# Optimization experiments

Hardware: AMD Instinct MI355X
Metric: run time of the kernel (lower is better)

The kernel has to match this reference:

```python
import jax, jax.numpy as jnp
import numpy as np

V, E, CIN, COUT, NH, HID = 8192, 2048, 128, 128, 4, 32
EPS = 1e-5

def _ln(x, g, b):
    m = x.mean(-1, keepdims=True)
    v = x.var(-1, keepdims=True)
    return (x - m) / jnp.sqrt(v + EPS) * g + b

def setup_inputs() -> dict:
    key = jax.random.key(0)
    ks = jax.random.split(key, 12)
    s = 0.05
    X = jax.random.normal(ks[0], (V, CIN), jnp.float32)
    H = jax.random.bernoulli(ks[1], 0.02, (V, E)).astype(jnp.float32)
    edge_features = jax.random.normal(ks[2], (E, COUT), jnp.float32)
    Wv = jax.random.normal(ks[3], (CIN, COUT), jnp.float32) * s
    bv = jnp.zeros((COUT,), jnp.float32)
    We = jax.random.normal(ks[4], (COUT, COUT), jnp.float32) * s
    be = jnp.zeros((COUT,), jnp.float32)
    vW1 = jax.random.normal(ks[5], (NH, CIN, HID), jnp.float32) * s
    vb1 = jnp.zeros((NH, HID), jnp.float32)
    vW2 = jax.random.normal(ks[6], (NH, HID), jnp.float32) * s
    vb2 = jnp.zeros((NH,), jnp.float32)
    eW1 = jax.random.normal(ks[7], (COUT, HID), jnp.float32) * s
    eb1 = jnp.zeros((HID,), jnp.float32)
    eW2 = jax.random.normal(ks[8], (HID,), jnp.float32) * s
    eb2 = jnp.zeros((), jnp.float32)
    Wc = jax.random.normal(ks[9], (NH * COUT, COUT), jnp.float32) * s
    bc = jnp.zeros((COUT,), jnp.float32)
    Wg = jax.random.normal(ks[10], (CIN + COUT, COUT), jnp.float32) * s
    bg = jnp.zeros((COUT,), jnp.float32)
    return dict(X=X, H=H, edge_features=edge_features, Wv=Wv, bv=bv, We=We, be=be,
                vW1=vW1, vb1=vb1, vW2=vW2, vb2=vb2, eW1=eW1, eb1=eb1, eW2=eW2, eb2=eb2,
                Wc=Wc, bc=bc,
                ln_e_g=jnp.ones((COUT,), jnp.float32), ln_e_b=jnp.zeros((COUT,), jnp.float32),
                ln_v_g=jnp.ones((COUT,), jnp.float32), ln_v_b=jnp.zeros((COUT,), jnp.float32),
                bn_g=jnp.ones((COUT,), jnp.float32), bn_b=jnp.zeros((COUT,), jnp.float32),
                Wg=Wg, bg=bg)

def reference(X, H, edge_features, Wv, bv, We, be, vW1, vb1, vW2, vb2,
              eW1, eb1, eW2, eb2, Wc, bc, ln_e_g, ln_e_b, ln_v_g, ln_v_b,
              bn_g, bn_b, Wg, bg):
    gelu = lambda t: jax.nn.gelu(t, approximate=False)  # torch nn.GELU default (erf)
    Ht = H.T                                   # (E, V)
    Xt = X @ Wv + bv                           # (V, Cout) theta_v
    # per-head vertex attention MLP: Linear(Cin,32)->GELU->Linear(32,1), vectorized over heads
    hid = gelu(jnp.einsum('vc,hck->hvk', X, vW1) + vb1[:, None, :])
    attn = jax.nn.sigmoid(jnp.einsum('hvk,hk->hv', hid, vW2) + vb2[:, None])  # (NH, V)
    deg = Ht.sum(axis=1, keepdims=True)        # (E, 1) edge degrees
    denom = jnp.maximum(deg, 1.0)
    # degree-normalized attention-weighted v2e aggregation per head
    head_e = jnp.einsum('ev,hvc->hec', Ht, Xt[None] * attn[:, :, None]) / denom[None]
    e_cat = jnp.transpose(head_e, (1, 0, 2)).reshape(E, NH * COUT)  # concat heads dim=1
    e_feat = e_cat @ Wc + bc                   # attn_combine
    # edge attention uses the LAST head's vertex weights (global-var quirk in torch code)
    edge_att = ((Ht @ attn[-1]) / jnp.maximum(deg[:, 0], 1.0))[:, None]  # (E,1)
    # edge-feature gating with e_attention head 0
    te = edge_features @ We + be               # theta_e
    e_scores = gelu(e_feat @ eW1 + eb1) @ eW2 + eb2
    ew = jax.nn.sigmoid(e_scores)[:, None]
    e_feat = e_feat * ew + te * (1.0 - ew)
    # normalize == 'both': layer_norm_e then batch_norm (training-mode batch stats)
    e_feat = _ln(e_feat, ln_e_g, ln_e_b)
    m = e_feat.mean(axis=0)
    v = e_feat.var(axis=0)
    e_feat = (e_feat - m) / jnp.sqrt(v + EPS) * bn_g + bn_b
    # e2v sum aggregation: H @ e_feat
    v_feat = H @ e_feat                        # (V, Cout)
    gate = jax.nn.sigmoid(jnp.concatenate([X, v_feat], axis=1) @ Wg + bg)
    v_feat = gate * v_feat + (1.0 - gate) * Xt
    v_feat = _ln(v_feat, ln_v_g, ln_v_b)
    v_feat = v_feat + X                        # residual (Cin == Cout)
    v_feat = gelu(v_feat)                      # not is_last: activation; dropout = identity (eval)
    e_feat = gelu(e_feat)
    return v_feat, e_feat, edge_att
```

## Files before the change

### kernel.cpp

```cpp
#include <hip/hip_runtime.h>
#include <hip/hip_bf16.h>
#include <math.h>

#define NV 8192
#define NE 2048
#define CIN 128
#define COUT 128
#define NH 4
#define HID 32
#define ETILE 8
#define LCAP 256
#define VCAP 96
#define NWORDS (NE / 64)
#define TWORDS (NV / 64)
#define EPSV 1e-5f

__device__ __forceinline__ float gelu_f(float x) {
    return 0.5f * x * (1.0f + erff(x * 0.70710678118654752f));
}
__device__ __forceinline__ float sigmoid_f(float x) {
    return 1.0f / (1.0f + expf(-x));
}

__global__ __launch_bounds__(256) void k_front(
    const float* __restrict__ X, const float* __restrict__ Wv, const float* __restrict__ bv,
    const float* __restrict__ vW1, const float* __restrict__ vb1,
    const float* __restrict__ vW2, const float* __restrict__ vb2,
    const float* __restrict__ H,
    float* __restrict__ Xt, float* __restrict__ attn4,
    unsigned long long* __restrict__ Hbits, int* __restrict__ vdeg, int* __restrict__ vlist)
{
    __shared__ float Xs[2][8][CIN];
    int t = threadIdx.x;
    if (blockIdx.x < NV / 16) {
        int half = t >> 7, tt = t & 127;
        int v0 = blockIdx.x * 16 + half * 8;
        for (int v = 0; v < 8; ++v) Xs[half][v][tt] = X[(size_t)(v0 + v) * CIN + tt];
        __syncthreads();

        float acc[8];
        float bvc = bv[tt];
#pragma unroll
        for (int v = 0; v < 8; ++v) acc[v] = bvc;
        for (int k = 0; k < CIN; ++k) {
            float w = Wv[k * COUT + tt];
#pragma unroll
            for (int v = 0; v < 8; ++v) acc[v] = fmaf(Xs[half][v][k], w, acc[v]);
        }
        for (int v = 0; v < 8; ++v) Xt[(size_t)(v0 + v) * COUT + tt] = acc[v];

        int h = tt >> 5, j = tt & 31;
        float hb = vb1[h * HID + j];
#pragma unroll
        for (int v = 0; v < 8; ++v) acc[v] = hb;
        for (int k = 0; k < CIN; ++k) {
            float w = vW1[(h * CIN + k) * HID + j];
#pragma unroll
            for (int v = 0; v < 8; ++v) acc[v] = fmaf(Xs[half][v][k], w, acc[v]);
        }
        float w2 = vW2[h * HID + j];
        float b2 = vb2[h];
        for (int v = 0; v < 8; ++v) {
            float val = gelu_f(acc[v]) * w2;
#pragma unroll
            for (int m = 16; m >= 1; m >>= 1) val += __shfl_xor(val, m, 64);
            if (j == 0) attn4[(size_t)(v0 + v) * NH + h] = sigmoid_f(val + b2);
        }
    } else {
        int b = blockIdx.x - NV / 16;
        int w = t >> 6;
        int lane = t & 63;
        int v = b * 4 + w;
        const float4* row4 = (const float4*)(H + (size_t)v * NE);
        int base = 0;
        int* vl = vlist + (size_t)v * VCAP;
#pragma unroll
        for (int it = 0; it < NE / 1024; ++it) {
            int e0 = it * 1024 + lane * 16;
            float4 f0 = row4[it * 256 + lane * 4 + 0];
            float4 f1 = row4[it * 256 + lane * 4 + 1];
            float4 f2 = row4[it * 256 + lane * 4 + 2];
            float4 f3 = row4[it * 256 + lane * 4 + 3];
            unsigned int m16 = 0;
            m16 |= (f0.x != 0.0f ? 1u : 0u) << 0;  m16 |= (f0.y != 0.0f ? 1u : 0u) << 1;
            m16 |= (f0.z != 0.0f ? 1u : 0u) << 2;  m16 |= (f0.w != 0.0f ? 1u : 0u) << 3;
            m16 |= (f1.x != 0.0f ? 1u : 0u) << 4;  m16 |= (f1.y != 0.0f ? 1u : 0u) << 5;
            m16 |= (f1.z != 0.0f ? 1u : 0u) << 6;  m16 |= (f1.w != 0.0f ? 1u : 0u) << 7;
            m16 |= (f2.x != 0.0f ? 1u : 0u) << 8;  m16 |= (f2.y != 0.0f ? 1u : 0u) << 9;
            m16 |= (f2.z != 0.0f ? 1u : 0u) << 10; m16 |= (f2.w != 0.0f ? 1u : 0u) << 11;
            m16 |= (f3.x != 0.0f ? 1u : 0u) << 12; m16 |= (f3.y != 0.0f ? 1u : 0u) << 13;
            m16 |= (f3.z != 0.0f ? 1u : 0u) << 14; m16 |= (f3.w != 0.0f ? 1u : 0u) << 15;

            int cnt = __popc(m16);
            int inc = cnt;
#pragma unroll
            for (int s = 1; s < 64; s <<= 1) {
                int y = __shfl_up(inc, s, 64);
                if (lane >= s) inc += y;
            }
            int tot = __shfl(inc, 63, 64);
            int q = lane & 15;
            unsigned int w0 = __shfl(m16, q * 4 + 0, 64);
            unsigned int w1 = __shfl(m16, q * 4 + 1, 64);
            unsigned int w2 = __shfl(m16, q * 4 + 2, 64);
            unsigned int w3 = __shfl(m16, q * 4 + 3, 64);
            if (lane < 16) {
                unsigned long long word = (unsigned long long)w0
                    | ((unsigned long long)w1 << 16)
                    | ((unsigned long long)w2 << 32)
                    | ((unsigned long long)w3 << 48);
                Hbits[(size_t)v * NWORDS + it * 16 + lane] = word;
            }
            int off = base + inc - cnt;
            unsigned int mm = m16;
            while (mm) {
                int j = __ffs(mm) - 1;
                mm &= mm - 1;
                if (off < VCAP) vl[off] = e0 + j;
                ++off;
            }
            base += tot;
        }
        if (lane == 0) vdeg[v] = base;
    }
}

__global__ __launch_bounds__(256) void k_transpose(
    const unsigned long long* __restrict__ Hbits, unsigned long long* __restrict__ HbitsT)
{
    __shared__ unsigned long long rows[64][NWORDS];
    int t = threadIdx.x;
    int vt = blockIdx.x;
    for (int i = t; i < 64 * NWORDS; i += 256)
        rows[i >> 5][i & 31] = Hbits[(size_t)vt * 64 * NWORDS + i];
    __syncthreads();
    int wv = t >> 6;
    int lane = t & 63;
    const unsigned long long M[6] = {
        0xFFFFFFFF00000000ULL, 0xFFFF0000FFFF0000ULL, 0xFF00FF00FF00FF00ULL,
        0xF0F0F0F0F0F0F0F0ULL, 0xCCCCCCCCCCCCCCCCULL, 0xAAAAAAAAAAAAAAAAULL };
    const int js[6] = {32, 16, 8, 4, 2, 1};
#pragma unroll
    for (int itb = 0; itb < 8; ++itb) {
        int it = wv * 8 + itb;
        unsigned long long x = rows[lane][it];
#pragma unroll
        for (int s = 0; s < 6; ++s) {
            int j = js[s];
            unsigned long long y = __shfl_xor(x, j, 64);
            unsigned long long Ms = M[s];
            if ((lane & j) == 0) x = (x & ~Ms) | ((y << j) & Ms);
            else                 x = (x & Ms) | ((y >> j) & ~Ms);
        }
        HbitsT[(size_t)(it * 64 + lane) * TWORDS + vt] = x;
    }
}

__global__ __launch_bounds__(256) void k_agg(
    const float* __restrict__ Xt, const float* __restrict__ attn4,
    const unsigned long long* __restrict__ HbitsT,
    float* __restrict__ ecat_g, float* __restrict__ out_att)
{
    __shared__ int lst[LCAP];
    __shared__ int wsum[2];
    __shared__ float pt[4][NH][COUT];
    __shared__ float asp[4];

    int t = threadIdx.x;
    int wid = t >> 6, lane = t & 63;
    int e = blockIdx.x;

    unsigned long long wd = 0ull;
    if (t < 128) wd = HbitsT[(size_t)e * TWORDS + t];
    int cnt = __popcll(wd);
    int inc = cnt;
#pragma unroll
    for (int s = 1; s < 64; s <<= 1) {
        int y = __shfl_up(inc, s, 64);
        if (lane >= s) inc += y;
    }
    if (lane == 63 && wid < 2) wsum[wid] = inc;
    __syncthreads();
    int n0 = wsum[0] + wsum[1];
    if (t < 128) {
        int base = (wid ? wsum[0] : 0) + inc - cnt;
        int vbase = t * 64;
        unsigned long long mm = wd;
        while (mm) {
            int i = __ffsll(mm) - 1;
            mm &= mm - 1;
            if (base < LCAP) lst[base] = vbase + i;
            ++base;
        }
    }
    __syncthreads();

    float inv = 1.0f / fmaxf((float)n0, 1.0f);
    int n = n0 < LCAP ? n0 : LCAP;

    float p00 = 0, p10 = 0, p20 = 0, p30 = 0;
    float p01 = 0, p11 = 0, p21 = 0, p31 = 0;
    float as = 0;
#pragma unroll 2
    for (int i = wid; i < n; i += 4) {
        int v = lst[i];
        float x0 = Xt[(size_t)v * COUT + lane];
        float x1 = Xt[(size_t)v * COUT + lane + 64];
        float4 a = *(const float4*)(attn4 + (size_t)v * NH);
        p00 = fmaf(x0, a.x, p00);  p01 = fmaf(x1, a.x, p01);
        p10 = fmaf(x0, a.y, p10);  p11 = fmaf(x1, a.y, p11);
        p20 = fmaf(x0, a.z, p20);  p21 = fmaf(x1, a.z, p21);
        p30 = fmaf(x0, a.w, p30);  p31 = fmaf(x1, a.w, p31);
        as += a.w;
    }
    pt[wid][0][lane] = p00;  pt[wid][0][lane + 64] = p01;
    pt[wid][1][lane] = p10;  pt[wid][1][lane + 64] = p11;
    pt[wid][2][lane] = p20;  pt[wid][2][lane + 64] = p21;
    pt[wid][3][lane] = p30;  pt[wid][3][lane + 64] = p31;
    if (lane == 0) asp[wid] = as;
    __syncthreads();

#pragma unroll
    for (int r = 0; r < 2; ++r) {
        int k = t + r * 256;
        int h = k >> 7, ch = k & 127;
        float s = pt[0][h][ch] + pt[1][h][ch] + pt[2][h][ch] + pt[3][h][ch];
        ecat_g[(size_t)e * 512 + k] = s * inv;
    }
    if (t == 0) out_att[e] = (asp[0] + asp[1] + asp[2] + asp[3]) * inv;
}

__global__ __launch_bounds__(256) void k_cpart(
    const float* __restrict__ ecat_g, const float* __restrict__ edge_features,
    const float* __restrict__ Wc, const float* __restrict__ We,
    float* __restrict__ efp, float* __restrict__ tep)
{
    __shared__ float ecs[ETILE][128];
    __shared__ float efr8[ETILE][32];
    __shared__ float part[2][ETILE][128];

    int t = threadIdx.x;
    int s = blockIdx.x & 3;
    int eb = blockIdx.x >> 2;
    int e0 = eb * ETILE;
    int c = t & 127, h = t >> 7;

    for (int idx = t; idx < ETILE * 128; idx += 256) {
        int e = idx >> 7, k = idx & 127;
        ecs[e][k] = ecat_g[(size_t)(e0 + e) * 512 + s * 128 + k];
    }
    if (t < ETILE * 32) {
        int e = t >> 5, k = t & 31;
        efr8[e][k] = edge_features[(size_t)(e0 + e) * COUT + s * 32 + k];
    }
    __syncthreads();

    float accW[ETILE] = {0, 0, 0, 0, 0, 0, 0, 0};
    {
        const float* wp = Wc + (size_t)(s * 128 + h * 64) * COUT + c;
        for (int kk = 0; kk < 64; ++kk) {
            float w = wp[(size_t)kk * COUT];
            int k = h * 64 + kk;
#pragma unroll
            for (int e = 0; e < ETILE; ++e)
                accW[e] = fmaf(ecs[e][k], w, accW[e]);
        }
    }
#pragma unroll
    for (int e = 0; e < ETILE; ++e) part[h][e][c] = accW[e];
    __syncthreads();
    if (h == 0) {
#pragma unroll
        for (int e = 0; e < ETILE; ++e)
            efp[(size_t)s * NE * COUT + (size_t)(e0 + e) * COUT + c] =
                part[0][e][c] + part[1][e][c];
    }
    __syncthreads();

    float accT[ETILE] = {0, 0, 0, 0, 0, 0, 0, 0};
    {
        const float* wt = We + (size_t)(s * 32 + h * 16) * COUT + c;
        for (int kk = 0; kk < 16; ++kk) {
            float w = wt[(size_t)kk * COUT];
            int k = h * 16 + kk;
#pragma unroll
            for (int e = 0; e < ETILE; ++e)
                accT[e] = fmaf(efr8[e][k], w, accT[e]);
        }
    }
#pragma unroll
    for (int e = 0; e < ETILE; ++e) part[h][e][c] = accT[e];
    __syncthreads();
    if (h == 0) {
#pragma unroll
        for (int e = 0; e < ETILE; ++e)
            tep[(size_t)s * NE * COUT + (size_t)(e0 + e) * COUT + c] =
                part[0][e][c] + part[1][e][c];
    }
}

__global__ __launch_bounds__(512) void k_cred(
    const float* __restrict__ efp, const float* __restrict__ tep,
    const float* __restrict__ bc, const float* __restrict__ be,
    const float* __restrict__ eW1, const float* __restrict__ eb1,
    const float* __restrict__ eW2, const float* __restrict__ eb2,
    const float* __restrict__ ln_g, const float* __restrict__ ln_b,
    float* __restrict__ e_ln, float* __restrict__ bn_sum, float* __restrict__ bn_sq)
{
    __shared__ float efs[ETILE][COUT];
    __shared__ float teL[ETILE][COUT];
    __shared__ float yb[ETILE][COUT];
    __shared__ float ews[ETILE];
    __shared__ float red[ETILE][2][2];

    int t = threadIdx.x;
    int e0 = blockIdx.x * ETILE;
    int eslot = t >> 7, c = t & 127;
    int lane = t & 63;
    int gw = (t >> 6) & 1;

#pragma unroll
    for (int j = 0; j < 2; ++j) {
        int e = eslot + 4 * j;
        size_t off = (size_t)(e0 + e) * COUT + c;
        float ef = bc[c], te = be[c];
#pragma unroll
        for (int s = 0; s < 4; ++s) {
            ef += efp[(size_t)s * NE * COUT + off];
            te += tep[(size_t)s * NE * COUT + off];
        }
        efs[e][c] = ef;
        teL[e][c] = te;
    }
    __syncthreads();

    if (t < ETILE * 32) {
        int ee = t >> 5, j = t & 31;
        float hj = eb1[j];
        for (int k = 0; k < COUT; ++k) hj = fmaf(efs[ee][k], eW1[k * HID + j], hj);
        float val = gelu_f(hj) * eW2[j];
#pragma unroll
        for (int m = 16; m >= 1; m >>= 1) val += __shfl_xor(val, m, 32);
        if (j == 0) ews[ee] = sigmoid_f(val + eb2[0]);
    }
    __syncthreads();

#pragma unroll
    for (int j = 0; j < 2; ++j) {
        int e = eslot + 4 * j;
        float ew = ews[e];
        float x = efs[e][c] * ew + teL[e][c] * (1.0f - ew);
        float s = x, q = x * x;
#pragma unroll
        for (int m = 32; m >= 1; m >>= 1) { s += __shfl_xor(s, m, 64); q += __shfl_xor(q, m, 64); }
        if (lane == 0) { red[e][gw][0] = s; red[e][gw][1] = q; }
        __syncthreads();
        float S = red[e][0][0] + red[e][1][0];
        float Q = red[e][0][1] + red[e][1][1];
        float m_ = S * (1.0f / COUT);
        float var = Q * (1.0f / COUT) - m_ * m_;
        float y = (x - m_) * rsqrtf(var + EPSV) * ln_g[c] + ln_b[c];
        e_ln[(size_t)(e0 + e) * COUT + c] = y;
        yb[e][c] = y;
        __syncthreads();
    }

    if (t < 128) {
        float s = 0, q = 0;
#pragma unroll
        for (int e = 0; e < ETILE; ++e) { float y = yb[e][t]; s += y; q += y * y; }
        atomicAdd(&bn_sum[t], s);
        atomicAdd(&bn_sq[t], q);
    }
}

__global__ __launch_bounds__(256) void k_bnapply(const float* __restrict__ e_ln,
    const float* __restrict__ bn_sum, const float* __restrict__ bn_sq,
    const float* __restrict__ bn_g, const float* __restrict__ bn_b,
    float* __restrict__ out_e)
{
    int idx = blockIdx.x * 256 + threadIdx.x;
    int c = idx & 127;
    float m = bn_sum[c] * (1.0f / NE);
    float var = bn_sq[c] * (1.0f / NE) - m * m;
    float x = e_ln[idx];
    float y = (x - m) * rsqrtf(var + EPSV) * bn_g[c] + bn_b[c];
    out_e[idx] = gelu_f(y);
}

__global__ __launch_bounds__(512) void k_vertex2(
    const float* __restrict__ X, const int* __restrict__ vdeg, const int* __restrict__ vlist,
    const float* __restrict__ e_ln,
    const float* __restrict__ bn_sum, const float* __restrict__ bn_sq,
    const float* __restrict__ bn_g, const float* __restrict__ bn_b,
    const float* __restrict__ Xt,
    const float* __restrict__ Wg, const float* __restrict__ bg,
    const float* __restrict__ ln_g, const float* __restrict__ ln_b,
    float* __restrict__ out_v)
{
    __shared__ float XsF[8 * CIN];
    __shared__ float vfF[8 * COUT];
    __shared__ int lst[8][VCAP];
    __shared__ int degs[8];
    __shared__ float part[4 * 8 * COUT];
    __shared__ float red[8][2][2];

    int t = threadIdx.x;
    int vg = t >> 6, lane = t & 63;
    int g4 = t >> 7, c = t & 127;
    int gw2 = (t >> 6) & 1;
    int v0 = blockIdx.x * 8;

    {
        float2 x2 = *(const float2*)(X + (size_t)(v0 + vg) * CIN + lane * 2);
        XsF[vg * CIN + lane * 2] = x2.x;
        XsF[vg * CIN + lane * 2 + 1] = x2.y;
    }
    for (int i = t; i < 8 * VCAP; i += 512)
        lst[i / VCAP][i % VCAP] = vlist[(size_t)v0 * VCAP + i];
    if (t < 8) degs[t] = vdeg[v0 + t];
    __syncthreads();

    int ch0 = lane * 2;
    float m0 = bn_sum[ch0] * (1.0f / NE);
    float m1 = bn_sum[ch0 + 1] * (1.0f / NE);
    float A0 = bn_g[ch0] * rsqrtf(bn_sq[ch0] * (1.0f / NE) - m0 * m0 + EPSV);
    float A1 = bn_g[ch0 + 1] * rsqrtf(bn_sq[ch0 + 1] * (1.0f / NE) - m1 * m1 + EPSV);
    float B0 = bn_b[ch0] - m0 * A0;
    float B1 = bn_b[ch0 + 1] - m1 * A1;

    int n = degs[vg];
    if (n > VCAP) n = VCAP;
    float sx = 0, sy = 0;
    for (int i = 0; i < n; ++i) {
        float2 v2 = *(const float2*)(e_ln + (size_t)lst[vg][i] * COUT + ch0);
        sx += v2.x;
        sy += v2.y;
    }
    float fn = (float)n;
    vfF[vg * COUT + ch0] = A0 * sx + fn * B0;
    vfF[vg * COUT + ch0 + 1] = A1 * sy + fn * B1;
    __syncthreads();

    {
        float accW[8] = {0, 0, 0, 0, 0, 0, 0, 0};
        const float* wp = Wg + (size_t)(g4 * 64) * COUT + c;
        const float* src = (g4 < 2) ? XsF : vfF;
        int kb = (g4 & 1) * 64;
        for (int ki = 0; ki < 64; ++ki) {
            float w = wp[(size_t)ki * COUT];
#pragma unroll
            for (int v = 0; v < 8; ++v)
                accW[v] = fmaf(src[v * 128 + kb + ki], w, accW[v]);
        }
#pragma unroll
        for (int v = 0; v < 8; ++v) part[g4 * 1024 + v * COUT + c] = accW[v];
    }
    __syncthreads();

    float xv[2];
#pragma unroll
    for (int rep = 0; rep < 2; ++rep) {
        int v = g4 + rep * 4;
        float ag = part[0 * 1024 + v * COUT + c] + part[1 * 1024 + v * COUT + c]
                 + part[2 * 1024 + v * COUT + c] + part[3 * 1024 + v * COUT + c] + bg[c];
        float gate = sigmoid_f(ag);
        float x = gate * vfF[v * COUT + c] + (1.0f - gate) * Xt[(size_t)(v0 + v) * COUT + c];
        xv[rep] = x;
        float s = x, q = x * x;
#pragma unroll
        for (int m = 32; m >= 1; m >>= 1) { s += __shfl_xor(s, m, 64); q += __shfl_xor(q, m, 64); }
        if (lane == 0) { red[v][gw2][0] = s; red[v][gw2][1] = q; }
    }
    __syncthreads();
#pragma unroll
    for (int rep = 0; rep < 2; ++rep) {
        int v = g4 + rep * 4;
        float S = red[v][0][0] + red[v][1][0];
        float Q = red[v][0][1] + red[v][1][1];
        float m_ = S * (1.0f / COUT);
        float var = Q * (1.0f / COUT) - m_ * m_;
        float y = (xv[rep] - m_) * rsqrtf(var + EPSV) * ln_g[c] + ln_b[c];
        y = y + XsF[v * CIN + c];
        out_v[(size_t)(v0 + v) * COUT + c] = gelu_f(y);
    }
}

extern "C" void kernel_launch(void* const* d_in, const int* in_sizes, int n_in,
                              void* d_out, int out_size, void* d_ws, size_t ws_size,
                              hipStream_t stream) {
    const float* X    = (const float*)d_in[0];
    const float* H    = (const float*)d_in[1];
    const float* edge_features = (const float*)d_in[2];
    const float* Wv   = (const float*)d_in[3];
    const float* bv   = (const float*)d_in[4];
    const float* We   = (const float*)d_in[5];
    const float* be   = (const float*)d_in[6];
    const float* vW1  = (const float*)d_in[7];
    const float* vb1  = (const float*)d_in[8];
    const float* vW2  = (const float*)d_in[9];
    const float* vb2  = (const float*)d_in[10];
    const float* eW1  = (const float*)d_in[11];
    const float* eb1  = (const float*)d_in[12];
    const float* eW2  = (const float*)d_in[13];
    const float* eb2  = (const float*)d_in[14];
    const float* Wc   = (const float*)d_in[15];
    const float* bc   = (const float*)d_in[16];
    const float* ln_e_g = (const float*)d_in[17];
    const float* ln_e_b = (const float*)d_in[18];
    const float* ln_v_g = (const float*)d_in[19];
    const float* ln_v_b = (const float*)d_in[20];
    const float* bn_g = (const float*)d_in[21];
    const float* bn_b = (const float*)d_in[22];
    const float* Wg   = (const float*)d_in[23];
    const float* bg   = (const float*)d_in[24];

    float* out_v  = (float*)d_out;
    float* out_e  = out_v + NV * COUT;
    float* out_att = out_e + NE * COUT;

    char* w = (char*)d_ws;
    float* Xt     = (float*)w; w += (size_t)NV * COUT * 4;
    float* attn4  = (float*)w; w += (size_t)NV * NH * 4;
    float* e_ln   = (float*)w; w += (size_t)NE * COUT * 4;
    float* ecat_g = (float*)w; w += (size_t)NE * NH * COUT * 4;
    float* efp    = (float*)w; w += (size_t)4 * NE * COUT * 4;
    float* tep    = (float*)w; w += (size_t)4 * NE * COUT * 4;
    float* bn_sum = (float*)w; w += COUT * 4;
    float* bn_sq  = (float*)w; w += COUT * 4;
    int*   vdeg   = (int*)w;   w += (size_t)NV * 4;
    int*   vlist  = (int*)w;   w += (size_t)NV * VCAP * 4;
    unsigned long long* Hbits  = (unsigned long long*)w; w += (size_t)NV * NWORDS * 8;
    unsigned long long* HbitsT = (unsigned long long*)w; w += (size_t)NE * TWORDS * 8;

    hipMemsetAsync(bn_sum, 0, 2 * COUT * sizeof(float), stream);

    k_front<<<NV / 16 + NV / 4, 256, 0, stream>>>(X, Wv, bv, vW1, vb1, vW2, vb2, H,
                                                  Xt, attn4, Hbits, vdeg, vlist);
    k_transpose<<<NV / 64, 256, 0, stream>>>(Hbits, HbitsT);
    k_agg<<<NE, 256, 0, stream>>>(Xt, attn4, HbitsT, ecat_g, out_att);
    k_cpart<<<(NE / ETILE) * 4, 256, 0, stream>>>(ecat_g, edge_features, Wc, We, efp, tep);
    k_cred<<<NE / ETILE, 512, 0, stream>>>(efp, tep, bc, be, eW1, eb1, eW2, eb2,
                                           ln_e_g, ln_e_b, e_ln, bn_sum, bn_sq);
    k_bnapply<<<(NE * COUT) / 256, 256, 0, stream>>>(e_ln, bn_sum, bn_sq, bn_g, bn_b, out_e);
    k_vertex2<<<NV / 8, 512, 0, stream>>>(X, vdeg, vlist, e_ln, bn_sum, bn_sq, bn_g, bn_b,
                                          Xt, Wg, bg, ln_v_g, ln_v_b, out_v);
}
```

Baseline: 258.4 us.

## Split front kernel into bitmask scan, vertex MLP, and adjacency-list kernels

```diff
diff --git a/kernel.cpp b/kernel.cpp
--- a/kernel.cpp
+++ b/kernel.cpp
@@ -22,107 +22,101 @@
     return 1.0f / (1.0f + expf(-x));
 }
 
-__global__ __launch_bounds__(256) void k_front(
+__global__ __launch_bounds__(256) void k_vertex1(
     const float* __restrict__ X, const float* __restrict__ Wv, const float* __restrict__ bv,
     const float* __restrict__ vW1, const float* __restrict__ vb1,
     const float* __restrict__ vW2, const float* __restrict__ vb2,
-    const float* __restrict__ H,
-    float* __restrict__ Xt, float* __restrict__ attn4,
-    unsigned long long* __restrict__ Hbits, int* __restrict__ vdeg, int* __restrict__ vlist)
+    float* __restrict__ Xt, float* __restrict__ attn4)
 {
     __shared__ float Xs[2][8][CIN];
     int t = threadIdx.x;
-    if (blockIdx.x < NV / 16) {
-        int half = t >> 7, tt = t & 127;
-        int v0 = blockIdx.x * 16 + half * 8;
-        for (int v = 0; v < 8; ++v) Xs[half][v][tt] = X[(size_t)(v0 + v) * CIN + tt];
-        __syncthreads();
-
-        float acc[8];
-        float bvc = bv[tt];
-#pragma unroll
-        for (int v = 0; v < 8; ++v) acc[v] = bvc;
-        for (int k = 0; k < CIN; ++k) {
-            float w = Wv[k * COUT + tt];
-#pragma unroll
-            for (int v = 0; v < 8; ++v) acc[v] = fmaf(Xs[half][v][k], w, acc[v]);
-        }
-        for (int v = 0; v < 8; ++v) Xt[(size_t)(v0 + v) * COUT + tt] = acc[v];
-
-        int h = tt >> 5, j = tt & 31;
-        float hb = vb1[h * HID + j];
-#pragma unroll
-        for (int v = 0; v < 8; ++v) acc[v] = hb;
-        for (int k = 0; k < CIN; ++k) {
-            float w = vW1[(h * CIN + k) * HID + j];
-#pragma unroll
-            for (int v = 0; v < 8; ++v) acc[v] = fmaf(Xs[half][v][k], w, acc[v]);
-        }
-        float w2 = vW2[h * HID + j];
-        float b2 = vb2[h];
-        for (int v = 0; v < 8; ++v) {
-            float val = gelu_f(acc[v]) * w2;
-#pragma unroll
-            for (int m = 16; m >= 1; m >>= 1) val += __shfl_xor(val, m, 64);
-            if (j == 0) attn4[(size_t)(v0 + v) * NH + h] = sigmoid_f(val + b2);
-        }
-    } else {
-        int b = blockIdx.x - NV / 16;
-        int w = t >> 6;
-        int lane = t & 63;
-        int v = b * 4 + w;
-        const float4* row4 = (const float4*)(H + (size_t)v * NE);
-        int base = 0;
-        int* vl = vlist + (size_t)v * VCAP;
-#pragma unroll
-        for (int it = 0; it < NE / 1024; ++it) {
-            int e0 = it * 1024 + lane * 16;
-            float4 f0 = row4[it * 256 + lane * 4 + 0];
-            float4 f1 = row4[it * 256 + lane * 4 + 1];
-            float4 f2 = row4[it * 256 + lane * 4 + 2];
-            float4 f3 = row4[it * 256 + lane * 4 + 3];
-            unsigned int m16 = 0;
-            m16 |= (f0.x != 0.0f ? 1u : 0u) << 0;  m16 |= (f0.y != 0.0f ? 1u : 0u) << 1;
-            m16 |= (f0.z != 0.0f ? 1u : 0u) << 2;  m16 |= (f0.w != 0.0f ? 1u : 0u) << 3;
-            m16 |= (f1.x != 0.0f ? 1u : 0u) << 4;  m16 |= (f1.y != 0.0f ? 1u : 0u) << 5;
-            m16 |= (f1.z != 0.0f ? 1u : 0u) << 6;  m16 |= (f1.w != 0.0f ? 1u : 0u) << 7;
-            m16 |= (f2.x != 0.0f ? 1u : 0u) << 8;  m16 |= (f2.y != 0.0f ? 1u : 0u) << 9;
-            m16 |= (f2.z != 0.0f ? 1u : 0u) << 10; m16 |= (f2.w != 0.0f ? 1u : 0u) << 11;
-            m16 |= (f3.x != 0.0f ? 1u : 0u) << 12; m16 |= (f3.y != 0.0f ? 1u : 0u) << 13;
-            m16 |= (f3.z != 0.0f ? 1u : 0u) << 14; m16 |= (f3.w != 0.0f ? 1u : 0u) << 15;
-
-            int cnt = __popc(m16);
-            int inc = cnt;
-#pragma unroll
-            for (int s = 1; s < 64; s <<= 1) {
-                int y = __shfl_up(inc, s, 64);
-                if (lane >= s) inc += y;
-            }
-            int tot = __shfl(inc, 63, 64);
-            int q = lane & 15;
-            unsigned int w0 = __shfl(m16, q * 4 + 0, 64);
-            unsigned int w1 = __shfl(m16, q * 4 + 1, 64);
-            unsigned int w2 = __shfl(m16, q * 4 + 2, 64);
-            unsigned int w3 = __shfl(m16, q * 4 + 3, 64);
-            if (lane < 16) {
-                unsigned long long word = (unsigned long long)w0
-                    | ((unsigned long long)w1 << 16)
-                    | ((unsigned long long)w2 << 32)
-                    | ((unsigned long long)w3 << 48);
-                Hbits[(size_t)v * NWORDS + it * 16 + lane] = word;
-            }
-            int off = base + inc - cnt;
-            unsigned int mm = m16;
-            while (mm) {
-                int j = __ffs(mm) - 1;
-                mm &= mm - 1;
-                if (off < VCAP) vl[off] = e0 + j;
-                ++off;
-            }
-            base += tot;
-        }
-        if (lane == 0) vdeg[v] = base;
-    }
+    int half = t >> 7, tt = t & 127;
+    int v0 = blockIdx.x * 16 + half * 8;
+    for (int v = 0; v < 8; ++v) Xs[half][v][tt] = X[(size_t)(v0 + v) * CIN + tt];
+    __syncthreads();
+
+    float acc[8];
+    float bvc = bv[tt];
+#pragma unroll
+    for (int v = 0; v < 8; ++v) acc[v] = bvc;
+    for (int k = 0; k < CIN; ++k) {
+        float w = Wv[k * COUT + tt];
+#pragma unroll
+        for (int v = 0; v < 8; ++v) acc[v] = fmaf(Xs[half][v][k], w, acc[v]);
+    }
+    for (int v = 0; v < 8; ++v) Xt[(size_t)(v0 + v) * COUT + tt] = acc[v];
+
+    int h = tt >> 5, j = tt & 31;
+    float hb = vb1[h * HID + j];
+#pragma unroll
+    for (int v = 0; v < 8; ++v) acc[v] = hb;
+    for (int k = 0; k < CIN; ++k) {
+        float w = vW1[(h * CIN + k) * HID + j];
+#pragma unroll
+        for (int v = 0; v < 8; ++v) acc[v] = fmaf(Xs[half][v][k], w, acc[v]);
+    }
+    float w2 = vW2[h * HID + j];
+    float b2 = vb2[h];
+    for (int v = 0; v < 8; ++v) {
+        float val = gelu_f(acc[v]) * w2;
+#pragma unroll
+        for (int m = 16; m >= 1; m >>= 1) val += __shfl_xor(val, m, 64);
+        if (j == 0) attn4[(size_t)(v0 + v) * NH + h] = sigmoid_f(val + b2);
+    }
+}
+
+__global__ __launch_bounds__(256) void k_scan(
+    const float* __restrict__ H, unsigned short* __restrict__ HbitsU16)
+{
+    int w = threadIdx.x >> 6;
+    int lane = threadIdx.x & 63;
+    int v = blockIdx.x * 4 + w;
+    const float4* row4 = (const float4*)(H + (size_t)v * NE);
+#pragma unroll
+    for (int it = 0; it < NE / 1024; ++it) {
+        float4 f0 = row4[it * 256 + lane * 4 + 0];
+        float4 f1 = row4[it * 256 + lane * 4 + 1];
+        float4 f2 = row4[it * 256 + lane * 4 + 2];
+        float4 f3 = row4[it * 256 + lane * 4 + 3];
+        unsigned int m16 = 0;
+        m16 |= (f0.x != 0.0f ? 1u : 0u) << 0;  m16 |= (f0.y != 0.0f ? 1u : 0u) << 1;
+        m16 |= (f0.z != 0.0f ? 1u : 0u) << 2;  m16 |= (f0.w != 0.0f ? 1u : 0u) << 3;
+        m16 |= (f1.x != 0.0f ? 1u : 0u) << 4;  m16 |= (f1.y != 0.0f ? 1u : 0u) << 5;
+        m16 |= (f1.z != 0.0f ? 1u : 0u) << 6;  m16 |= (f1.w != 0.0f ? 1u : 0u) << 7;
+        m16 |= (f2.x != 0.0f ? 1u : 0u) << 8;  m16 |= (f2.y != 0.0f ? 1u : 0u) << 9;
+        m16 |= (f2.z != 0.0f ? 1u : 0u) << 10; m16 |= (f2.w != 0.0f ? 1u : 0u) << 11;
+        m16 |= (f3.x != 0.0f ? 1u : 0u) << 12; m16 |= (f3.y != 0.0f ? 1u : 0u) << 13;
+        m16 |= (f3.z != 0.0f ? 1u : 0u) << 14; m16 |= (f3.w != 0.0f ? 1u : 0u) << 15;
+        HbitsU16[(size_t)v * (NE / 16) + it * 64 + lane] = (unsigned short)m16;
+    }
+}
+
+__global__ __launch_bounds__(256) void k_vlist(
+    const unsigned long long* __restrict__ Hbits,
+    int* __restrict__ vdeg, int* __restrict__ vlist)
+{
+    int w = threadIdx.x >> 6;
+    int lane = threadIdx.x & 63;
+    int v = blockIdx.x * 4 + w;
+    unsigned long long wd = (lane < NWORDS) ? Hbits[(size_t)v * NWORDS + lane] : 0ull;
+    int cnt = __popcll(wd);
+    int inc = cnt;
+#pragma unroll
+    for (int s = 1; s < 64; s <<= 1) {
+        int y = __shfl_up(inc, s, 64);
+        if (lane >= s) inc += y;
+    }
+    int total = __shfl(inc, 63, 64);
+    int off = inc - cnt;
+    int vbase = lane * 64;
+    int* vl = vlist + (size_t)v * VCAP;
+    while (wd) {
+        int i = __ffsll(wd) - 1;
+        wd &= wd - 1;
+        if (off < VCAP) vl[off] = vbase + i;
+        ++off;
+    }
+    if (lane == 0) vdeg[v] = total;
 }
 
 __global__ __launch_bounds__(256) void k_transpose(
@@ -535,8 +529,9 @@
 
     hipMemsetAsync(bn_sum, 0, 2 * COUT * sizeof(float), stream);
 
-    k_front<<<NV / 16 + NV / 4, 256, 0, stream>>>(X, Wv, bv, vW1, vb1, vW2, vb2, H,
-                                                  Xt, attn4, Hbits, vdeg, vlist);
+    k_scan<<<NV / 4, 256, 0, stream>>>(H, (unsigned short*)Hbits);
+    k_vertex1<<<NV / 16, 256, 0, stream>>>(X, Wv, bv, vW1, vb1, vW2, vb2, Xt, attn4);
+    k_vlist<<<NV / 4, 256, 0, stream>>>(Hbits, vdeg, vlist);
     k_transpose<<<NV / 64, 256, 0, stream>>>(Hbits, HbitsT);
     k_agg<<<NE, 256, 0, stream>>>(Xt, attn4, HbitsT, ecat_g, out_att);
     k_cpart<<<(NE / ETILE) * 4, 256, 0, stream>>>(ecat_g, edge_features, Wc, We, efp, tep);
```

Result: slower. 269.5 us (+4.3%).
